# Kernel tuning notes

Hardware: AMD Instinct MI355X
Metric: run time of the kernel (lower is better)

Reference implementation:

```python
import jax, jax.numpy as jnp
import numpy as np

UPS_MEL = 100   # mel frame -> samples
UPS_LOW = 10    # lowres -> samples
H = 512         # GRU hidden
MEL = 80
LC = 20         # lowres conv channels
PRE = 256
SS = 30         # MOL sample_size (10 mixtures x 3)


def setup_inputs() -> dict:
    key = jax.random.key(0)
    ks = jax.random.split(key, 16)
    B, TM, TL = 8, 80, 800
    T = TM * UPS_MEL  # 8000
    rn = lambda k, s, sc=1.0: jax.random.normal(k, s, dtype=jnp.float32) * sc
    z = lambda n: jnp.zeros((n,), dtype=jnp.float32)
    return {
        "mel": rn(ks[0], (B, TM, MEL)),
        "x_low": rn(ks[1], (B, TL), 0.5),
        "gs_x": rn(ks[2], (B, T), 0.5),
        "conv_w0": rn(ks[3], (LC, 1, 7), 0.3),
        "conv_b0": z(LC),
        "conv_w1": rn(ks[4], (LC, LC, 7), 0.1),
        "conv_b1": z(LC),
        "conv_w2": rn(ks[5], (LC, LC, 7), 0.1),
        "conv_b2": z(LC),
        "gru_wih0": rn(ks[6], (3 * H, 102), 0.05),
        "gru_whh0": rn(ks[7], (3 * H, H), 0.05),
        "gru_bih0": z(3 * H),
        "gru_bhh0": z(3 * H),
        "gru_wih1": rn(ks[8], (3 * H, H), 0.05),
        "gru_whh1": rn(ks[9], (3 * H, H), 0.05),
        "gru_bih1": z(3 * H),
        "gru_bhh1": z(3 * H),
        "pre_w": rn(ks[10], (PRE, H), 0.05),
        "pre_b": z(PRE),
        "out_w": rn(ks[11], (SS, PRE), 0.05),
        "out_b": z(SS),
    }


def _lin_interp(x, out_len):
    # torch F.interpolate(mode='linear', align_corners=False) on [B, L] -> [B, out_len]
    L = x.shape[1]
    src = (jnp.arange(out_len, dtype=jnp.float32) + 0.5) * (L / out_len) - 0.5
    src = jnp.clip(src, 0.0, L - 1)
    i0 = jnp.floor(src).astype(jnp.int32)
    i1 = jnp.minimum(i0 + 1, L - 1)
    w = src - i0.astype(jnp.float32)
    return x[:, i0] * (1.0 - w) + x[:, i1] * w


def _conv1d(x, w, b):
    # x: [B, C, L], w: [O, I, K], 'same' padding (K=7 -> pad 3)
    k = w.shape[-1]
    p = (k - 1) // 2
    y = jax.lax.conv_general_dilated(x, w, (1,), [(p, p)],
                                     dimension_numbers=("NCH", "OIH", "NCH"))
    return y + b[None, :, None]


def _gru(x, wih, whh, bih, bhh):
    # x: [B, T, I] -> [B, T, H]; PyTorch GRU gate math, h0 = 0
    B = x.shape[0]
    xg = jnp.einsum("bti,gi->btg", x, wih) + bih  # [B, T, 3H]
    h0 = jnp.zeros((B, H), dtype=x.dtype)

    def step(h, xg_t):
        hg = h @ whh.T + bhh
        xr, xz, xn = jnp.split(xg_t, 3, axis=-1)
        hr, hz, hn = jnp.split(hg, 3, axis=-1)
        r = jax.nn.sigmoid(xr + hr)
        z = jax.nn.sigmoid(xz + hz)
        n = jnp.tanh(xn + r * hn)
        h_new = (1.0 - z) * n + z * h
        return h_new, h_new

    _, hs = jax.lax.scan(step, h0, jnp.swapaxes(xg, 0, 1))
    return jnp.swapaxes(hs, 0, 1)


def reference(mel, x_low, gs_x,
              conv_w0, conv_b0, conv_w1, conv_b1, conv_w2, conv_b2,
              gru_wih0, gru_whh0, gru_bih0, gru_bhh0,
              gru_wih1, gru_whh1, gru_bih1, gru_bhh1,
              pre_w, pre_b, out_w, out_b):
    # UpsampleNetR on mel: repeat each frame UPS_MEL times -> [B, T, 80]
    up_mel = jnp.repeat(mel, UPS_MEL, axis=1)
    # UpsampleNetI on x_low: linear interp x UPS_LOW -> [B, TL*10]
    interp_x = _lin_interp(x_low, x_low.shape[1] * UPS_LOW)
    # lowres conv stack with tanh: [B, 1, TL] -> [B, 20, TL]
    h = x_low[:, None, :]
    for w, b in ((conv_w0, conv_b0), (conv_w1, conv_b1), (conv_w2, conv_b2)):
        h = jnp.tanh(_conv1d(h, w, b))
    # UpsampleNetR on conv features: [B, TL, 20] repeated x10 -> [B, TL*10, 20]
    up_x = jnp.repeat(jnp.swapaxes(h, 1, 2), UPS_LOW, axis=1)

    msize = min(up_mel.shape[1], gs_x.shape[1], up_x.shape[1], interp_x.shape[1])
    hidden = jnp.concatenate([up_mel[:, :msize, :], up_x[:, :msize, :],
                              interp_x[:, :msize, None], gs_x[:, :msize, None]],
                             axis=-1)  # [B, T, 102]

    hidden = _gru(hidden, gru_wih0, gru_whh0, gru_bih0, gru_bhh0)
    hidden = _gru(hidden, gru_wih1, gru_whh1, gru_bih1, gru_bhh1)

    pre = jnp.tanh(hidden @ pre_w.T + pre_b)   # [B, T, 256]
    return pre @ out_w.T + out_b               # [B, T, 30]
```

## Files before the change

kernel.cpp:

```cpp
#include <hip/hip_runtime.h>
#include <hip/hip_fp16.h>
#include <stdint.h>

#define TT     8000
#define TLOW   800
#define TMEL   80
#define NMEL   80
#define NB     8
#define HD     512
#define LC     20
#define NPRE   256
#define NSS    30

#define HB_SLOTS (TT + 1)
#define HB_U64   ((size_t)HB_SLOTS * 8 * 128)
#define HB_BYTES (HB_U64 * 8)
#define CONV_BYTES   ((size_t)NB * TLOW * LC * 4)
#define INTERP_BYTES ((size_t)NB * TT * 4)
#define PREW16_BYTES ((size_t)NPRE * HD * 2)
#define OUTW16_BYTES ((size_t)NSS * NPRE * 2)

typedef __attribute__((ext_vector_type(8))) _Float16 half8;
typedef __attribute__((ext_vector_type(4))) float f32x4;

static __device__ __forceinline__ unsigned short f2h_bits(float f) {
    union { _Float16 h; unsigned short u; } c; c.h = (_Float16)f; return c.u;
}
static __device__ __forceinline__ float sigf(float x) {
    x = fminf(30.f, fmaxf(-30.f, x));
    return 1.f / (1.f + __expf(-x));
}
static __device__ __forceinline__ float tanhf_(float x) {
    x = fminf(15.f, fmaxf(-15.f, x));
    float e = __expf(2.f * x);
    return (e - 1.f) / (e + 1.f);
}
static __device__ __forceinline__ half8 mkfrag(unsigned long long a, unsigned long long b) {
    union { unsigned long long q[2]; half8 v; } u; u.q[0] = a; u.q[1] = b; return u.v;
}
static __device__ __forceinline__ f32x4 mfma(half8 a, half8 b, f32x4 c) {
    return __builtin_amdgcn_mfma_f32_16x16x32_f16(a, b, c, 0, 0, 0);
}

static __device__ __forceinline__ void poll_stage(const unsigned long long* __restrict__ slot,
                                                  int lane, unsigned long long* __restrict__ st)
{
    unsigned long long v[16];
    for (;;) {
        #pragma unroll
        for (int k = 0; k < 16; k++)
            v[k] = __hip_atomic_load(slot + lane + 64 * k, __ATOMIC_RELAXED, __HIP_MEMORY_SCOPE_AGENT);
        bool bad = false;
        #pragma unroll
        for (int k = 0; k < 16; k++) {
            unsigned int lo = (unsigned int)v[k], hi = (unsigned int)(v[k] >> 32);
            bad |= (lo == 0xFFFFFFFFu) | (hi == 0xFFFFFFFFu);
        }
        if (!__any(bad)) break;
        __builtin_amdgcn_s_sleep(1);
    }
    #pragma unroll
    for (int k = 0; k < 16; k++) {
        int i = lane + 64 * k;
        st[(i >> 7) * 129 + (i & 127)] = v[k];
    }
}
static __device__ __forceinline__ half8 ldsfrag(const unsigned long long* __restrict__ st,
                                                int lane, int kt)
{
    int base = (lane & 7) * 129 + ((lane >> 4) << 1) + kt * 8;
    return mkfrag(st[base], st[base + 1]);
}

__global__ __launch_bounds__(256) void k_prep(
    const float* __restrict__ pre_w, const float* __restrict__ out_w,
    unsigned short* __restrict__ prew16, unsigned short* __restrict__ outw16)
{
    int i = blockIdx.x * 256 + threadIdx.x;
    if (i < NPRE * HD) prew16[i] = f2h_bits(pre_w[i]);
    if (i < NSS * NPRE) outw16[i] = f2h_bits(out_w[i]);
}

#define CHW 218
__global__ __launch_bounds__(256) void k_conv(
    const float* __restrict__ xlow,
    const float* __restrict__ w0, const float* __restrict__ cb0,
    const float* __restrict__ w1, const float* __restrict__ cb1,
    const float* __restrict__ w2, const float* __restrict__ cb2,
    float* __restrict__ convout, float* __restrict__ interp)
{
    int blk = blockIdx.x; int b = blk >> 2; int ch = blk & 3; int cb = ch * 200;
    int tid = threadIdx.x;
    __shared__ float xr[224];
    __shared__ float w0l[LC * 7], w1l[LC * LC * 7], w2l[LC * LC * 7];
    __shared__ float b0l[LC], b1l[LC], b2l[LC];
    __shared__ float h0[LC][CHW], h1[LC][CHW];

    for (int i = tid; i < LC * 7; i += 256) w0l[i] = w0[i];
    for (int i = tid; i < LC * LC * 7; i += 256) { w1l[i] = w1[i]; w2l[i] = w2[i]; }
    for (int i = tid; i < LC; i += 256) { b0l[i] = cb0[i]; b1l[i] = cb1[i]; b2l[i] = cb2[i]; }
    for (int i = tid; i < 224; i += 256) {
        int g = cb - 12 + i;
        xr[i] = (g >= 0 && g < TLOW) ? xlow[b * TLOW + g] : 0.f;
    }
    __syncthreads();
    for (int i = tid; i < LC * CHW; i += 256) {
        int c = i / CHW, s = i - c * CHW;
        int tg = cb - 9 + s;
        float a = b0l[c];
        #pragma unroll
        for (int j = 0; j < 7; j++) a += w0l[c * 7 + j] * xr[s + j];
        h0[c][s] = (tg >= 0 && tg < TLOW) ? tanhf_(a) : 0.f;
    }
    __syncthreads();
    for (int i = tid; i < LC * CHW; i += 256) {
        int c = i / CHW, s = i - c * CHW;
        int tg = cb - 9 + s;
        float a = b1l[c];
        for (int ci = 0; ci < LC; ci++) {
            #pragma unroll
            for (int j = 0; j < 7; j++) {
                int ss = s + j - 3;
                float hv = (ss >= 0 && ss < CHW) ? h0[ci][ss] : 0.f;
                a += w1l[(c * LC + ci) * 7 + j] * hv;
            }
        }
        h1[c][s] = (tg >= 0 && tg < TLOW) ? tanhf_(a) : 0.f;
    }
    __syncthreads();
    for (int i = tid; i < LC * 200; i += 256) {
        int c = i / 200, t0 = i - c * 200; int s = t0 + 9;
        float a = b2l[c];
        for (int ci = 0; ci < LC; ci++) {
            #pragma unroll
            for (int j = 0; j < 7; j++) a += w2l[(c * LC + ci) * 7 + j] * h1[ci][s + j - 3];
        }
        convout[((size_t)b * TLOW + cb + t0) * LC + c] = tanhf_(a);
    }
    for (int i = tid; i < 2000; i += 256) {
        int t = cb * 10 + i;
        float src = ((float)t + 0.5f) * 0.1f - 0.5f;
        src = fminf(fmaxf(src, 0.f), (float)(TLOW - 1));
        int i0 = (int)floorf(src); int i1 = (i0 + 1 < TLOW) ? i0 + 1 : TLOW - 1;
        float w = src - (float)i0;
        interp[(size_t)b * TT + t] = xlow[b * TLOW + i0] * (1.f - w) + xlow[b * TLOW + i1] * w;
    }
}

__global__ __launch_bounds__(192, 1) void k_rnn(
    const float* __restrict__ mel, const float* __restrict__ gsx,
    const float* __restrict__ convout, const float* __restrict__ interp,
    const float* __restrict__ wih0, const float* __restrict__ whh0,
    const float* __restrict__ bih0, const float* __restrict__ bhh0,
    const float* __restrict__ wih1, const float* __restrict__ whh1,
    const float* __restrict__ bih1, const float* __restrict__ bhh1,
    unsigned long long* __restrict__ h0buf, unsigned long long* __restrict__ h1buf)
{
    const int tid = threadIdx.x;
    const int wv = tid >> 6;
    const int lane = tid & 63;
    const int lm = lane & 15, lk = lane >> 4;
    const bool isL0 = (blockIdx.x < 32);
    const int cbid = isL0 ? blockIdx.x : (blockIdx.x - 32);
    const int cb = cbid * 16;
    const int row = wv * 512 + cb + lm;

    __shared__ float exch[3][2][16][9];
    __shared__ __align__(16) unsigned short xvec[16][136];
    __shared__ unsigned long long stX[8 * 129];
    __shared__ unsigned long long stH[8 * 129];

    const int cbb = lane >> 3;
    const int ci0 = (lane & 7) * 2, ci1 = ci0 + 1;
    float hr0 = 0.f, hr1 = 0.f;
    float bi0[3], bi1[3], bh0[3], bh1[3];
    {
        const float* bi = isL0 ? bih0 : bih1;
        const float* bh = isL0 ? bhh0 : bhh1;
        #pragma unroll
        for (int g = 0; g < 3; g++) {
            bi0[g] = bi[g * 512 + cb + ci0]; bi1[g] = bi[g * 512 + cb + ci1];
            bh0[g] = bh[g * 512 + cb + ci0]; bh1[g] = bh[g * 512 + cb + ci1];
        }
    }
    for (int i = tid; i < 16 * 136; i += 192) (&xvec[0][0])[i] = 0;

    {
        unsigned long long* buf = isL0 ? h0buf : h1buf;
        if (wv == 0) {
            unsigned int* o32 = (unsigned int*)buf + (size_t)cbb * 256 + (cb >> 1) + (lane & 7);
            __hip_atomic_store(o32, 0u, __ATOMIC_RELAXED, __HIP_MEMORY_SCOPE_AGENT);
        }
    }

    if (isL0) {
        half8 wf[20];
        #pragma unroll
        for (int kt = 0; kt < 20; kt++) {
            #pragma unroll
            for (int j = 0; j < 8; j++) {
                int k = kt * 32 + lk * 8 + j;
                float v;
                if (kt < 4) v = (k < 102) ? wih0[(size_t)row * 102 + k] : 0.f;
                else        v = whh0[(size_t)row * 512 + (k - 128)];
                wf[kt][j] = (_Float16)v;
            }
        }
        {
            float pf[5];
            #pragma unroll
            for (int u = 0; u < 5; u++) {
                int e = tid + 192 * u; float v = 0.f;
                if (e < 816) {
                    int bb = e / 102, k = e - 102 * bb;
                    if (k < 80)       v = mel[((size_t)bb * TMEL + 0) * NMEL + k];
                    else if (k < 100) v = convout[((size_t)bb * TLOW + 0) * LC + (k - 80)];
                    else if (k == 100) v = interp[(size_t)bb * TT + 0];
                    else               v = gsx[(size_t)bb * TT + 0];
                }
                pf[u] = v;
            }
            #pragma unroll
            for (int u = 0; u < 5; u++) {
                int e = tid + 192 * u;
                if (e < 816) { int bb = e / 102, k = e - 102 * bb; xvec[bb][k] = f2h_bits(pf[u]); }
            }
        }
        __syncthreads();

        for (int t = 0; t < TT; t++) {
            int tn = (t + 1 < TT) ? (t + 1) : (TT - 1);
            int tmi = tn / 100, tli = tn / 10;
            float pf[5];
            #pragma unroll
            for (int u = 0; u < 5; u++) {
                int e = tid + 192 * u; float v = 0.f;
                if (e < 816) {
                    int bb = e / 102, k = e - 102 * bb;
                    if (k < 80)       v = mel[((size_t)bb * TMEL + tmi) * NMEL + k];
                    else if (k < 100) v = convout[((size_t)bb * TLOW + tli) * LC + (k - 80)];
                    else if (k == 100) v = interp[(size_t)bb * TT + tn];
                    else               v = gsx[(size_t)bb * TT + tn];
                }
                pf[u] = v;
            }

            if (wv == 0) poll_stage(h0buf + (size_t)t * 1024, lane, stH);
            __syncthreads();

            f32x4 accX = {0.f, 0.f, 0.f, 0.f};
            #pragma unroll
            for (int kt = 0; kt < 4; kt++) {
                half8 xf = *(const half8*)&xvec[lm][kt * 32 + lk * 8];
                accX = mfma(wf[kt], xf, accX);
            }
            f32x4 a0 = {0.f, 0.f, 0.f, 0.f}, a1 = {0.f, 0.f, 0.f, 0.f};
            #pragma unroll
            for (int i = 0; i < 8; i++) a0 = mfma(wf[4 + i], ldsfrag(stH, lane, i), a0);
            #pragma unroll
            for (int i = 0; i < 8; i++) a1 = mfma(wf[12 + i], ldsfrag(stH, lane, 8 + i), a1);
            f32x4 accH = a0 + a1;

            if (lm < 8) {
                #pragma unroll
                for (int r2 = 0; r2 < 4; r2++) {
                    exch[wv][0][lk * 4 + r2][lm] = accX[r2];
                    exch[wv][1][lk * 4 + r2][lm] = accH[r2];
                }
            }
            __syncthreads();
            if (wv == 0) {
                float Xr0 = exch[0][0][ci0][cbb], Hr0 = exch[0][1][ci0][cbb];
                float Xz0 = exch[1][0][ci0][cbb], Hz0 = exch[1][1][ci0][cbb];
                float Xn0 = exch[2][0][ci0][cbb], Hn0 = exch[2][1][ci0][cbb];
                float r0 = sigf(Xr0 + Hr0 + bi0[0] + bh0[0]);
                float z0 = sigf(Xz0 + Hz0 + bi0[1] + bh0[1]);
                float n0 = tanhf_(Xn0 + bi0[2] + r0 * (Hn0 + bh0[2]));
                hr0 = (1.f - z0) * n0 + z0 * hr0;
                float Xr1 = exch[0][0][ci1][cbb], Hr1 = exch[0][1][ci1][cbb];
                float Xz1 = exch[1][0][ci1][cbb], Hz1 = exch[1][1][ci1][cbb];
                float Xn1 = exch[2][0][ci1][cbb], Hn1 = exch[2][1][ci1][cbb];
                float r1 = sigf(Xr1 + Hr1 + bi1[0] + bh1[0]);
                float z1 = sigf(Xz1 + Hz1 + bi1[1] + bh1[1]);
                float n1 = tanhf_(Xn1 + bi1[2] + r1 * (Hn1 + bh1[2]));
                hr1 = (1.f - z1) * n1 + z1 * hr1;
                unsigned int pk = (unsigned int)f2h_bits(hr0) | ((unsigned int)f2h_bits(hr1) << 16);
                unsigned int* o32 = (unsigned int*)(h0buf + (size_t)(t + 1) * 1024)
                                  + (size_t)cbb * 256 + (cb >> 1) + (lane & 7);
                __hip_atomic_store(o32, pk, __ATOMIC_RELAXED, __HIP_MEMORY_SCOPE_AGENT);
            }
            #pragma unroll
            for (int u = 0; u < 5; u++) {
                int e = tid + 192 * u;
                if (e < 816) { int bb = e / 102, k = e - 102 * bb; xvec[bb][k] = f2h_bits(pf[u]); }
            }
            __syncthreads();
        }
    } else {
        half8 wf[32];
        #pragma unroll
        for (int kt = 0; kt < 32; kt++) {
            #pragma unroll
            for (int j = 0; j < 8; j++) {
                int k = kt * 32 + lk * 8 + j;
                float v = (kt < 16) ? wih1[(size_t)row * 512 + k]
                                    : whh1[(size_t)row * 512 + (k - 512)];
                wf[kt][j] = (_Float16)v;
            }
        }
        __syncthreads();

        for (int t = 0; t < TT; t++) {
            if (wv == 0)      poll_stage(h0buf + (size_t)(t + 1) * 1024, lane, stX);
            else if (wv == 1) poll_stage(h1buf + (size_t)t * 1024,       lane, stH);
            __syncthreads();

            f32x4 x0 = {0.f, 0.f, 0.f, 0.f}, x1 = {0.f, 0.f, 0.f, 0.f};
            #pragma unroll
            for (int i = 0; i < 8; i++) x0 = mfma(wf[i],     ldsfrag(stX, lane, i),     x0);
            #pragma unroll
            for (int i = 0; i < 8; i++) x1 = mfma(wf[8 + i], ldsfrag(stX, lane, 8 + i), x1);
            f32x4 accX = x0 + x1;
            f32x4 a0 = {0.f, 0.f, 0.f, 0.f}, a1 = {0.f, 0.f, 0.f, 0.f};
            #pragma unroll
            for (int i = 0; i < 8; i++) a0 = mfma(wf[16 + i], ldsfrag(stH, lane, i),     a0);
            #pragma unroll
            for (int i = 0; i < 8; i++) a1 = mfma(wf[24 + i], ldsfrag(stH, lane, 8 + i), a1);
            f32x4 accH = a0 + a1;

            if (lm < 8) {
                #pragma unroll
                for (int r2 = 0; r2 < 4; r2++) {
                    exch[wv][0][lk * 4 + r2][lm] = accX[r2];
                    exch[wv][1][lk * 4 + r2][lm] = accH[r2];
                }
            }
            __syncthreads();
            if (wv == 0) {
                float Xr0 = exch[0][0][ci0][cbb], Hr0 = exch[0][1][ci0][cbb];
                float Xz0 = exch[1][0][ci0][cbb], Hz0 = exch[1][1][ci0][cbb];
                float Xn0 = exch[2][0][ci0][cbb], Hn0 = exch[2][1][ci0][cbb];
                float r0 = sigf(Xr0 + Hr0 + bi0[0] + bh0[0]);
                float z0 = sigf(Xz0 + Hz0 + bi0[1] + bh0[1]);
                float n0 = tanhf_(Xn0 + bi0[2] + r0 * (Hn0 + bh0[2]));
                hr0 = (1.f - z0) * n0 + z0 * hr0;
                float Xr1 = exch[0][0][ci1][cbb], Hr1 = exch[0][1][ci1][cbb];
                float Xz1 = exch[1][0][ci1][cbb], Hz1 = exch[1][1][ci1][cbb];
                float Xn1 = exch[2][0][ci1][cbb], Hn1 = exch[2][1][ci1][cbb];
                float r1 = sigf(Xr1 + Hr1 + bi1[0] + bh1[0]);
                float z1 = sigf(Xz1 + Hz1 + bi1[1] + bh1[1]);
                float n1 = tanhf_(Xn1 + bi1[2] + r1 * (Hn1 + bh1[2]));
                hr1 = (1.f - z1) * n1 + z1 * hr1;
                unsigned int pk = (unsigned int)f2h_bits(hr0) | ((unsigned int)f2h_bits(hr1) << 16);
                unsigned int* o32 = (unsigned int*)(h1buf + (size_t)(t + 1) * 1024)
                                  + (size_t)cbb * 256 + (cb >> 1) + (lane & 7);
                __hip_atomic_store(o32, pk, __ATOMIC_RELAXED, __HIP_MEMORY_SCOPE_AGENT);
            }
            __syncthreads();
        }
    }
}

__global__ __launch_bounds__(256) void k_final(
    const unsigned long long* __restrict__ h1buf,
    const unsigned short* __restrict__ prew16, const float* __restrict__ pre_b,
    const unsigned short* __restrict__ outw16, const float* __restrict__ out_b,
    float* __restrict__ out)
{
    int blk = blockIdx.x; int b = blk / 125; int tb = (blk - b * 125) * 64;
    int tid = threadIdx.x; int wv = tid >> 6; int l = tid & 63;
    int lm = l & 15, lk = l >> 4;

    half8 af[16];
    int trow = tb + wv * 16 + lm;
    const unsigned long long* abase = h1buf + ((size_t)(trow + 1) * 8 + b) * 128;
    #pragma unroll
    for (int kt = 0; kt < 16; kt++)
        af[kt] = mkfrag(abase[kt * 8 + lk * 2], abase[kt * 8 + lk * 2 + 1]);

    f32x4 acc[16];
    #pragma unroll
    for (int nt = 0; nt < 16; nt++) {
        f32x4 z = {0.f, 0.f, 0.f, 0.f}; acc[nt] = z;
        #pragma unroll
        for (int kt = 0; kt < 16; kt++) {
            int n = nt * 16 + lm; int k = kt * 32 + lk * 8;
            half8 bw = *(const half8*)&prew16[(size_t)n * HD + k];
            acc[nt] = mfma(af[kt], bw, acc[nt]);
        }
    }
    __shared__ __align__(16) unsigned short pt[64][264];
    #pragma unroll
    for (int nt = 0; nt < 16; nt++) {
        float pb = pre_b[nt * 16 + lm];
        #pragma unroll
        for (int r2 = 0; r2 < 4; r2++)
            pt[wv * 16 + lk * 4 + r2][nt * 16 + lm] = f2h_bits(tanhf_(acc[nt][r2] + pb));
    }
    __syncthreads();
    f32x4 a2[2];
    { f32x4 z = {0.f, 0.f, 0.f, 0.f}; a2[0] = z; a2[1] = z; }
    #pragma unroll
    for (int kt = 0; kt < 8; kt++) {
        half8 pa = *(const half8*)&pt[wv * 16 + lm][kt * 32 + lk * 8];
        #pragma unroll
        for (int nt = 0; nt < 2; nt++) {
            int n = nt * 16 + lm;
            half8 bw = (n < NSS) ? *(const half8*)&outw16[(size_t)n * NPRE + kt * 32 + lk * 8]
                                 : mkfrag(0ull, 0ull);
            a2[nt] = mfma(pa, bw, a2[nt]);
        }
    }
    #pragma unroll
    for (int nt = 0; nt < 2; nt++) {
        int n = nt * 16 + lm;
        if (n < NSS) {
            float ob = out_b[n];
            #pragma unroll
            for (int r2 = 0; r2 < 4; r2++) {
                int t = tb + wv * 16 + lk * 4 + r2;
                out[((size_t)b * TT + t) * NSS + n] = a2[nt][r2] + ob;
            }
        }
    }
}

extern "C" void kernel_launch(void* const* d_in, const int* in_sizes, int n_in,
                              void* d_out, int out_size, void* d_ws, size_t ws_size,
                              hipStream_t stream) {
    const float* mel  = (const float*)d_in[0];
    const float* xlow = (const float*)d_in[1];
    const float* gsx  = (const float*)d_in[2];
    const float* cw0  = (const float*)d_in[3];
    const float* cb0  = (const float*)d_in[4];
    const float* cw1  = (const float*)d_in[5];
    const float* cb1  = (const float*)d_in[6];
    const float* cw2  = (const float*)d_in[7];
    const float* cb2  = (const float*)d_in[8];
    const float* wih0 = (const float*)d_in[9];
    const float* whh0 = (const float*)d_in[10];
    const float* bih0 = (const float*)d_in[11];
    const float* bhh0 = (const float*)d_in[12];
    const float* wih1 = (const float*)d_in[13];
    const float* whh1 = (const float*)d_in[14];
    const float* bih1 = (const float*)d_in[15];
    const float* bhh1 = (const float*)d_in[16];
    const float* prew = (const float*)d_in[17];
    const float* preb = (const float*)d_in[18];
    const float* outw = (const float*)d_in[19];
    const float* outb = (const float*)d_in[20];

    size_t needed = 2 * HB_BYTES + CONV_BYTES + INTERP_BYTES + PREW16_BYTES + OUTW16_BYTES;
    if (ws_size < needed) return;

    char* ws = (char*)d_ws;
    unsigned long long* h0buf = (unsigned long long*)ws;
    unsigned long long* h1buf = (unsigned long long*)(ws + HB_BYTES);
    float* convout = (float*)(ws + 2 * HB_BYTES);
    float* interp  = (float*)(ws + 2 * HB_BYTES + CONV_BYTES);
    unsigned short* prew16 = (unsigned short*)(ws + 2 * HB_BYTES + CONV_BYTES + INTERP_BYTES);
    unsigned short* outw16 = (unsigned short*)(ws + 2 * HB_BYTES + CONV_BYTES + INTERP_BYTES + PREW16_BYTES);

    hipMemsetAsync(ws, 0xFF, 2 * HB_BYTES, stream);

    k_prep<<<(NPRE * HD + 255) / 256, 256, 0, stream>>>(prew, outw, prew16, outw16);
    k_conv<<<32, 256, 0, stream>>>(xlow, cw0, cb0, cw1, cb1, cw2, cb2, convout, interp);
    k_rnn<<<64, 192, 0, stream>>>(mel, gsx, convout, interp,
                                  wih0, whh0, bih0, bhh0,
                                  wih1, whh1, bih1, bhh1,
                                  h0buf, h1buf);
    k_final<<<1000, 256, 0, stream>>>(h1buf, prew16, preb, outw16, outb, (float*)d_out);
}
```

Baseline: 20.28 ms.

## Consolidate GRU recurrence into 16 larger blocks of 12 waves each

The persistent GRU kernel moves from 64 blocks of 3 waves, each owning 16 hidden units, to 16 blocks of 12 waves, each owning 64 hidden units. Each layer now uses 8 cooperating blocks instead of 32. Gate math is done by two waves, each handling 4 units per lane, and the hidden state is published as 64-bit stores. The aim is to cut the number of blocks that must poll and synchronise through global memory at every timestep, at the cost of larger intra-block barriers and fewer CUs in use.

```diff
diff --git a/kernel.cpp b/kernel.cpp
--- a/kernel.cpp
+++ b/kernel.cpp
@@ -147,7 +147,7 @@
     }
 }
 
-__global__ __launch_bounds__(192, 1) void k_rnn(
+__global__ __launch_bounds__(768, 1) void k_rnn(
     const float* __restrict__ mel, const float* __restrict__ gsx,
     const float* __restrict__ convout, const float* __restrict__ interp,
     const float* __restrict__ wih0, const float* __restrict__ whh0,
@@ -160,37 +160,40 @@
     const int wv = tid >> 6;
     const int lane = tid & 63;
     const int lm = lane & 15, lk = lane >> 4;
-    const bool isL0 = (blockIdx.x < 32);
-    const int cbid = isL0 ? blockIdx.x : (blockIdx.x - 32);
-    const int cb = cbid * 16;
-    const int row = wv * 512 + cb + lm;
-
-    __shared__ float exch[3][2][16][9];
+    const bool isL0 = (blockIdx.x < 8);
+    const int cbid = isL0 ? blockIdx.x : (blockIdx.x - 8);
+    const int cb = cbid * 64;
+    const int g  = wv >> 2, ti = wv & 3;
+    const int row = g * 512 + cb + ti * 16 + lm;
+
+    __shared__ float exch[3][2][64][9];
     __shared__ __align__(16) unsigned short xvec[16][136];
     __shared__ unsigned long long stX[8 * 129];
     __shared__ unsigned long long stH[8 * 129];
 
     const int cbb = lane >> 3;
-    const int ci0 = (lane & 7) * 2, ci1 = ci0 + 1;
-    float hr0 = 0.f, hr1 = 0.f;
-    float bi0[3], bi1[3], bh0[3], bh1[3];
+    const int ci0 = wv * 32 + (lane & 7) * 4;
+    float hr[4] = {0.f, 0.f, 0.f, 0.f};
+    float bi[3][4], bh[3][4];
     {
-        const float* bi = isL0 ? bih0 : bih1;
-        const float* bh = isL0 ? bhh0 : bhh1;
-        #pragma unroll
-        for (int g = 0; g < 3; g++) {
-            bi0[g] = bi[g * 512 + cb + ci0]; bi1[g] = bi[g * 512 + cb + ci1];
-            bh0[g] = bh[g * 512 + cb + ci0]; bh1[g] = bh[g * 512 + cb + ci1];
-        }
-    }
-    for (int i = tid; i < 16 * 136; i += 192) (&xvec[0][0])[i] = 0;
-
-    {
+        const float* bip = isL0 ? bih0 : bih1;
+        const float* bhp = isL0 ? bhh0 : bhh1;
+        int i0c = (wv < 2) ? ci0 : 0;
+        #pragma unroll
+        for (int gg = 0; gg < 3; gg++)
+            #pragma unroll
+            for (int e = 0; e < 4; e++) {
+                bi[gg][e] = bip[gg * 512 + cb + i0c + e];
+                bh[gg][e] = bhp[gg * 512 + cb + i0c + e];
+            }
+    }
+    for (int i = tid; i < 16 * 136; i += 768) (&xvec[0][0])[i] = 0;
+
+    if (wv < 2) {
         unsigned long long* buf = isL0 ? h0buf : h1buf;
-        if (wv == 0) {
-            unsigned int* o32 = (unsigned int*)buf + (size_t)cbb * 256 + (cb >> 1) + (lane & 7);
-            __hip_atomic_store(o32, 0u, __ATOMIC_RELAXED, __HIP_MEMORY_SCOPE_AGENT);
-        }
+        int word = 16 * cbid + 8 * wv + (lane & 7);
+        __hip_atomic_store(buf + (size_t)cbb * 128 + word, 0ull,
+                           __ATOMIC_RELAXED, __HIP_MEMORY_SCOPE_AGENT);
     }
 
     if (isL0) {
@@ -207,10 +210,10 @@
             }
         }
         {
-            float pf[5];
-            #pragma unroll
-            for (int u = 0; u < 5; u++) {
-                int e = tid + 192 * u; float v = 0.f;
+            float pf[2];
+            #pragma unroll
+            for (int u = 0; u < 2; u++) {
+                int e = tid + 768 * u; float v = 0.f;
                 if (e < 816) {
                     int bb = e / 102, k = e - 102 * bb;
                     if (k < 80)       v = mel[((size_t)bb * TMEL + 0) * NMEL + k];
@@ -221,8 +224,8 @@
                 pf[u] = v;
             }
             #pragma unroll
-            for (int u = 0; u < 5; u++) {
-                int e = tid + 192 * u;
+            for (int u = 0; u < 2; u++) {
+                int e = tid + 768 * u;
                 if (e < 816) { int bb = e / 102, k = e - 102 * bb; xvec[bb][k] = f2h_bits(pf[u]); }
             }
         }
@@ -231,10 +234,10 @@
         for (int t = 0; t < TT; t++) {
             int tn = (t + 1 < TT) ? (t + 1) : (TT - 1);
             int tmi = tn / 100, tli = tn / 10;
-            float pf[5];
-            #pragma unroll
-            for (int u = 0; u < 5; u++) {
-                int e = tid + 192 * u; float v = 0.f;
+            float pf[2];
+            #pragma unroll
+            for (int u = 0; u < 2; u++) {
+                int e = tid + 768 * u; float v = 0.f;
                 if (e < 816) {
                     int bb = e / 102, k = e - 102 * bb;
                     if (k < 80)       v = mel[((size_t)bb * TMEL + tmi) * NMEL + k];
@@ -264,34 +267,29 @@
             if (lm < 8) {
                 #pragma unroll
                 for (int r2 = 0; r2 < 4; r2++) {
-                    exch[wv][0][lk * 4 + r2][lm] = accX[r2];
-                    exch[wv][1][lk * 4 + r2][lm] = accH[r2];
-                }
-            }
-            __syncthreads();
-            if (wv == 0) {
-                float Xr0 = exch[0][0][ci0][cbb], Hr0 = exch[0][1][ci0][cbb];
-                float Xz0 = exch[1][0][ci0][cbb], Hz0 = exch[1][1][ci0][cbb];
-                float Xn0 = exch[2][0][ci0][cbb], Hn0 = exch[2][1][ci0][cbb];
-                float r0 = sigf(Xr0 + Hr0 + bi0[0] + bh0[0]);
-                float z0 = sigf(Xz0 + Hz0 + bi0[1] + bh0[1]);
-                float n0 = tanhf_(Xn0 + bi0[2] + r0 * (Hn0 + bh0[2]));
-                hr0 = (1.f - z0) * n0 + z0 * hr0;
-                float Xr1 = exch[0][0][ci1][cbb], Hr1 = exch[0][1][ci1][cbb];
-                float Xz1 = exch[1][0][ci1][cbb], Hz1 = exch[1][1][ci1][cbb];
-                float Xn1 = exch[2][0][ci1][cbb], Hn1 = exch[2][1][ci1][cbb];
-                float r1 = sigf(Xr1 + Hr1 + bi1[0] + bh1[0]);
-                float z1 = sigf(Xz1 + Hz1 + bi1[1] + bh1[1]);
-                float n1 = tanhf_(Xn1 + bi1[2] + r1 * (Hn1 + bh1[2]));
-                hr1 = (1.f - z1) * n1 + z1 * hr1;
-                unsigned int pk = (unsigned int)f2h_bits(hr0) | ((unsigned int)f2h_bits(hr1) << 16);
-                unsigned int* o32 = (unsigned int*)(h0buf + (size_t)(t + 1) * 1024)
-                                  + (size_t)cbb * 256 + (cb >> 1) + (lane & 7);
-                __hip_atomic_store(o32, pk, __ATOMIC_RELAXED, __HIP_MEMORY_SCOPE_AGENT);
-            }
-            #pragma unroll
-            for (int u = 0; u < 5; u++) {
-                int e = tid + 192 * u;
+                    exch[g][0][ti * 16 + lk * 4 + r2][lm] = accX[r2];
+                    exch[g][1][ti * 16 + lk * 4 + r2][lm] = accH[r2];
+                }
+            }
+            __syncthreads();
+            if (wv < 2) {
+                unsigned long long pk = 0ull;
+                #pragma unroll
+                for (int e = 0; e < 4; e++) {
+                    int i = ci0 + e;
+                    float r = sigf(exch[0][0][i][cbb] + exch[0][1][i][cbb] + bi[0][e] + bh[0][e]);
+                    float z = sigf(exch[1][0][i][cbb] + exch[1][1][i][cbb] + bi[1][e] + bh[1][e]);
+                    float n = tanhf_(exch[2][0][i][cbb] + bi[2][e] + r * (exch[2][1][i][cbb] + bh[2][e]));
+                    hr[e] = (1.f - z) * n + z * hr[e];
+                    pk |= ((unsigned long long)f2h_bits(hr[e])) << (16 * e);
+                }
+                int word = 16 * cbid + 8 * wv + (lane & 7);
+                __hip_atomic_store(h0buf + (size_t)(t + 1) * 1024 + (size_t)cbb * 128 + word, pk,
+                                   __ATOMIC_RELAXED, __HIP_MEMORY_SCOPE_AGENT);
+            }
+            #pragma unroll
+            for (int u = 0; u < 2; u++) {
+                int e = tid + 768 * u;
                 if (e < 816) { int bb = e / 102, k = e - 102 * bb; xvec[bb][k] = f2h_bits(pf[u]); }
             }
             __syncthreads();
@@ -331,30 +329,25 @@
             if (lm < 8) {
                 #pragma unroll
                 for (int r2 = 0; r2 < 4; r2++) {
-                    exch[wv][0][lk * 4 + r2][lm] = accX[r2];
-                    exch[wv][1][lk * 4 + r2][lm] = accH[r2];
-                }
-            }
-            __syncthreads();
-            if (wv == 0) {
-                float Xr0 = exch[0][0][ci0][cbb], Hr0 = exch[0][1][ci0][cbb];
-                float Xz0 = exch[1][0][ci0][cbb], Hz0 = exch[1][1][ci0][cbb];
-                float Xn0 = exch[2][0][ci0][cbb], Hn0 = exch[2][1][ci0][cbb];
-                float r0 = sigf(Xr0 + Hr0 + bi0[0] + bh0[0]);
-                float z0 = sigf(Xz0 + Hz0 + bi0[1] + bh0[1]);
-                float n0 = tanhf_(Xn0 + bi0[2] + r0 * (Hn0 + bh0[2]));
-                hr0 = (1.f - z0) * n0 + z0 * hr0;
-                float Xr1 = exch[0][0][ci1][cbb], Hr1 = exch[0][1][ci1][cbb];
-                float Xz1 = exch[1][0][ci1][cbb], Hz1 = exch[1][1][ci1][cbb];
-                float Xn1 = exch[2][0][ci1][cbb], Hn1 = exch[2][1][ci1][cbb];
-                float r1 = sigf(Xr1 + Hr1 + bi1[0] + bh1[0]);
-                float z1 = sigf(Xz1 + Hz1 + bi1[1] + bh1[1]);
-                float n1 = tanhf_(Xn1 + bi1[2] + r1 * (Hn1 + bh1[2]));
-                hr1 = (1.f - z1) * n1 + z1 * hr1;
-                unsigned int pk = (unsigned int)f2h_bits(hr0) | ((unsigned int)f2h_bits(hr1) << 16);
-                unsigned int* o32 = (unsigned int*)(h1buf + (size_t)(t + 1) * 1024)
-                                  + (size_t)cbb * 256 + (cb >> 1) + (lane & 7);
-                __hip_atomic_store(o32, pk, __ATOMIC_RELAXED, __HIP_MEMORY_SCOPE_AGENT);
+                    exch[g][0][ti * 16 + lk * 4 + r2][lm] = accX[r2];
+                    exch[g][1][ti * 16 + lk * 4 + r2][lm] = accH[r2];
+                }
+            }
+            __syncthreads();
+            if (wv < 2) {
+                unsigned long long pk = 0ull;
+                #pragma unroll
+                for (int e = 0; e < 4; e++) {
+                    int i = ci0 + e;
+                    float r = sigf(exch[0][0][i][cbb] + exch[0][1][i][cbb] + bi[0][e] + bh[0][e]);
+                    float z = sigf(exch[1][0][i][cbb] + exch[1][1][i][cbb] + bi[1][e] + bh[1][e]);
+                    float n = tanhf_(exch[2][0][i][cbb] + bi[2][e] + r * (exch[2][1][i][cbb] + bh[2][e]));
+                    hr[e] = (1.f - z) * n + z * hr[e];
+                    pk |= ((unsigned long long)f2h_bits(hr[e])) << (16 * e);
+                }
+                int word = 16 * cbid + 8 * wv + (lane & 7);
+                __hip_atomic_store(h1buf + (size_t)(t + 1) * 1024 + (size_t)cbb * 128 + word, pk,
+                                   __ATOMIC_RELAXED, __HIP_MEMORY_SCOPE_AGENT);
             }
             __syncthreads();
         }
@@ -465,7 +458,7 @@
 
     k_prep<<<(NPRE * HD + 255) / 256, 256, 0, stream>>>(prew, outw, prew16, outw16);
     k_conv<<<32, 256, 0, stream>>>(xlow, cw0, cb0, cw1, cb1, cw2, cb2, convout, interp);
-    k_rnn<<<64, 192, 0, stream>>>(mel, gsx, convout, interp,
+    k_rnn<<<16, 768, 0, stream>>>(mel, gsx, convout, interp,
                                   wih0, whh0, bih0, bhh0,
                                   wih1, whh1, bih1, bhh1,
                                   h0buf, h1buf);
```

Result: slower. 53.98 ms (+166.2%).
